# Kernel tuning notes

Hardware: AMD Instinct MI355X
Metric: run time of the kernel (lower is better)

Reference implementation:

```python
import jax, jax.numpy as jnp
import numpy as np

E, S, Q, NN_NODES, R = 2048, 256, 25, 36, 15
H = 128  # MLP hidden width


def setup_inputs() -> dict:
    key = jax.random.key(0)
    ks = jax.random.split(key, 16)
    g = lambda k, shape, scale=1.0: (jax.random.normal(k, shape, dtype=jnp.float32) * scale)
    inp = {
        "nodes": g(ks[0], (E, NN_NODES, 2)),
        "W1": g(ks[1], (2, H), 1.0 / np.sqrt(2.0)),
        "b1": jnp.zeros((H,), jnp.float32),
        "W2": g(ks[2], (H, H), 1.0 / np.sqrt(H)),
        "b2": jnp.zeros((H,), jnp.float32),
        "W3": g(ks[3], (H, H), 1.0 / np.sqrt(H)),
        "b3": jnp.zeros((H,), jnp.float32),
        "W4": g(ks[4], (H, 1), 1.0 / np.sqrt(H)),
        "b4": jnp.zeros((1,), jnp.float32),
        # 2nd-derivative interpolation matrices of the inter basis B at the
        # sub-element quadrature points (shared across big elements).
        "Ixx": g(ks[5], (S, Q, NN_NODES), 0.1),
        "Iyy": g(ks[6], (S, Q, NN_NODES), 0.1),
        # per-big-element 2x2 Hessian change-of-coordinates map (B_DD_inter)
        "B_DD": g(ks[7], (E, 2, 2)),
        "w_quad": jax.random.uniform(ks[8], (Q,), dtype=jnp.float32),
        # test-function values at quadrature points (b.Base)
        "Base": g(ks[9], (Q, R)),
        # per-sub-element Jacobians and precomputed RHS projections F_total
        "J": jax.random.uniform(ks[10], (E, S), dtype=jnp.float32),
        "F": g(ks[11], (E, S, R)),
    }
    return inp


def _mlp(x, W1, b1, W2, b2, W3, b3, W4, b4):
    h = jnp.tanh(x @ W1 + b1)
    h = jnp.tanh(h @ W2 + b2)
    h = jnp.tanh(h @ W3 + b3)
    return h @ W4 + b4


def reference(nodes, W1, b1, W2, b2, W3, b3, W4, b4,
              Ixx, Iyy, B_DD, w_quad, Base, J, F):
    # NN evaluated once per big element at its interpolation nodes: [E, n_nodes]
    ev = _mlp(nodes.reshape(-1, 2), W1, b1, W2, b2, W3, b3, W4, b4)
    ev = ev.reshape(E, NN_NODES)
    d2x = jnp.einsum("sqn,en->esq", Ixx, ev)
    d2y = jnp.einsum("sqn,en->esq", Iyy, ev)
    grad_second = jnp.stack([d2x, d2y], axis=2)           # [E,S,2,Q]
    # B_DD_inter @ grad_second^T, per big element
    grad_second = jnp.einsum("eij,esjq->esiq", B_DD, grad_second)
    integrand_1 = grad_second.sum(axis=2)                 # [E,S,Q]
    # u_NN_el[r] = -J * sum_q w[q] * Base[q,r] * integrand_1[q]
    u_el = -J[:, :, None] * jnp.einsum("q,qr,esq->esr", w_quad, Base, integrand_1)
    res = u_el - F                                        # [E,S,R]
    # loss_element = mean over test functions, summed over all (big, sub) elements
    return jnp.sum(jnp.mean(jnp.square(res), axis=-1))
```

## Files before the change

### kernel.cpp

```cpp
#include <hip/hip_runtime.h>

#define EN 2048
#define SN 256
#define QN 25
#define NNODES 36
#define RN 15
#define HN 128

typedef __attribute__((ext_vector_type(8))) short short8;
typedef __attribute__((ext_vector_type(4))) float f32x4;
typedef __attribute__((ext_vector_type(2))) unsigned int uint2v;

__device__ __forceinline__ unsigned short f2bf(float f) {
    unsigned int u = __float_as_uint(f);
    u += 0x7fffu + ((u >> 16) & 1u);
    return (unsigned short)(u >> 16);
}
__device__ __forceinline__ float bf2f(unsigned short h) {
    return __uint_as_float(((unsigned int)h) << 16);
}
__device__ __forceinline__ float fast_tanh(float x) {
    float xs = x * 2.885390082f;
    xs = fminf(fmaxf(xs, -60.f), 60.f);
    float e = __builtin_amdgcn_exp2f(xs);
    float r = __builtin_amdgcn_rcpf(e + 1.f);
    return fmaf(-2.f, r, 1.f);
}

__global__ void zero_kernel(float* __restrict__ out) {
    if (threadIdx.x == 0) out[0] = 0.f;
}

__global__ __launch_bounds__(256)
void mc_kernel(const float* __restrict__ Ixx, const float* __restrict__ Iyy,
               const float* __restrict__ wq, const float* __restrict__ Base,
               float* __restrict__ Mc)
{
    __shared__ float WB[QN * 16];
    const int t = threadIdx.x;
    for (int i = t; i < QN * 16; i += 256) {
        const int q = i >> 4, r = i & 15;
        if (r < RN) WB[i] = wq[q] * Base[q * RN + r];
    }
    __syncthreads();
    const int o = blockIdx.x * 256 + t;
    const int c  = o % 72;
    const int sr = o / 72;
    const int r  = sr % RN;
    const int s  = sr / RN;
    const float* __restrict__ I = (c < NNODES) ? Ixx : Iyy;
    const int n = (c < NNODES) ? c : (c - NNODES);
    float a0 = 0.f, a1 = 0.f;
    #pragma unroll
    for (int q = 0; q < QN - 1; q += 2) {
        a0 = fmaf(WB[q * 16 + r],       I[(s * QN + q) * NNODES + n],       a0);
        a1 = fmaf(WB[(q + 1) * 16 + r], I[(s * QN + q + 1) * NNODES + n],   a1);
    }
    a0 = fmaf(WB[(QN - 1) * 16 + r], I[(s * QN + QN - 1) * NNODES + n], a0);
    Mc[o] = a0 + a1;
}

__device__ __forceinline__ void load_W(const float* __restrict__ W,
                                       unsigned short (*Ws)[136], int t)
{
    const int n = t & 127;
    const int h = t >> 7;
    #pragma unroll
    for (int kk = 0; kk < 16; kk++) {
        const int k0 = (kk * 2 + h) * 4;
        const float a0 = W[(k0 + 0) * HN + n];
        const float a1 = W[(k0 + 1) * HN + n];
        const float a2 = W[(k0 + 2) * HN + n];
        const float a3 = W[(k0 + 3) * HN + n];
        uint2v pk;
        pk[0] = (unsigned)f2bf(a0) | ((unsigned)f2bf(a1) << 16);
        pk[1] = (unsigned)f2bf(a2) | ((unsigned)f2bf(a3) << 16);
        *(uint2v*)&Ws[n][k0] = pk;
    }
}

__device__ __forceinline__ void mfma_layer(unsigned short (*Hs)[136],
                                           const unsigned short (*Ws)[136],
                                           const float* __restrict__ bias,
                                           int wv, int rowA, int quad)
{
    const int r0 = wv * 32;
    short8 afrag[2][4];
    #pragma unroll
    for (int rt = 0; rt < 2; rt++)
        #pragma unroll
        for (int kt = 0; kt < 4; kt++)
            afrag[rt][kt] = *(const short8*)&Hs[r0 + rt * 16 + rowA][kt * 32 + quad * 8];

    f32x4 acc[2][8];
    const f32x4 zero = {0.f, 0.f, 0.f, 0.f};
    #pragma unroll
    for (int rt = 0; rt < 2; rt++)
        #pragma unroll
        for (int nt = 0; nt < 8; nt++) acc[rt][nt] = zero;

    #pragma unroll
    for (int nt = 0; nt < 8; nt++) {
        #pragma unroll
        for (int kt = 0; kt < 4; kt++) {
            const short8 bfrag = *(const short8*)&Ws[nt * 16 + rowA][kt * 32 + quad * 8];
            acc[0][nt] = __builtin_amdgcn_mfma_f32_16x16x32_bf16(afrag[0][kt], bfrag, acc[0][nt], 0, 0, 0);
            acc[1][nt] = __builtin_amdgcn_mfma_f32_16x16x32_bf16(afrag[1][kt], bfrag, acc[1][nt], 0, 0, 0);
        }
    }
    #pragma unroll
    for (int nt = 0; nt < 8; nt++) {
        const int col = nt * 16 + rowA;
        const float bv = bias[col];
        #pragma unroll
        for (int rt = 0; rt < 2; rt++) {
            #pragma unroll
            for (int rg = 0; rg < 4; rg++) {
                const float v = fast_tanh(acc[rt][nt][rg] + bv);
                Hs[r0 + rt * 16 + quad * 4 + rg][col] = f2bf(v);
            }
        }
    }
}

__global__ __launch_bounds__(256, 2)
void mlp_kernel(const float* __restrict__ nodes,
                const float* __restrict__ W1, const float* __restrict__ b1,
                const float* __restrict__ W2, const float* __restrict__ b2,
                const float* __restrict__ W3, const float* __restrict__ b3,
                const float* __restrict__ W4, const float* __restrict__ b4,
                const float* __restrict__ B_DD,
                float* __restrict__ evc)
{
    __shared__ unsigned short Hs[128][136];
    __shared__ unsigned short Ws[128][136];
    const int t    = threadIdx.x;
    const int lane = t & 63;
    const int wv   = t >> 6;
    const int rowA = lane & 15;
    const int quad = lane >> 4;

    {
        const int p  = t >> 1;
        const int P  = blockIdx.x * 128 + p;
        const float x0 = nodes[2 * P], x1 = nodes[2 * P + 1];
        const int n0 = (t & 1) * 64;
        #pragma unroll
        for (int i = 0; i < 16; i++) {
            const int n = n0 + 4 * i;
            const float4 wa = *(const float4*)(W1 + n);
            const float4 wb = *(const float4*)(W1 + HN + n);
            const float4 bb = *(const float4*)(b1 + n);
            const float h0 = fast_tanh(fmaf(x0, wa.x, fmaf(x1, wb.x, bb.x)));
            const float h1 = fast_tanh(fmaf(x0, wa.y, fmaf(x1, wb.y, bb.y)));
            const float h2 = fast_tanh(fmaf(x0, wa.z, fmaf(x1, wb.z, bb.z)));
            const float h3 = fast_tanh(fmaf(x0, wa.w, fmaf(x1, wb.w, bb.w)));
            uint2v pk;
            pk[0] = (unsigned)f2bf(h0) | ((unsigned)f2bf(h1) << 16);
            pk[1] = (unsigned)f2bf(h2) | ((unsigned)f2bf(h3) << 16);
            *(uint2v*)&Hs[p][n] = pk;
        }
    }
    load_W(W2, Ws, t);
    __syncthreads();
    mfma_layer(Hs, Ws, b2, wv, rowA, quad);
    __syncthreads();
    load_W(W3, Ws, t);
    __syncthreads();
    mfma_layer(Hs, Ws, b3, wv, rowA, quad);
    {
        const int p  = t >> 1;
        const int k0 = (t & 1) * 64;
        float d = 0.f;
        #pragma unroll
        for (int i = 0; i < 8; i++) {
            const short8 h = *(const short8*)&Hs[p][k0 + 8 * i];
            const float4 wA = *(const float4*)(W4 + k0 + 8 * i);
            const float4 wB = *(const float4*)(W4 + k0 + 8 * i + 4);
            d = fmaf(bf2f((unsigned short)h[0]), wA.x, d);
            d = fmaf(bf2f((unsigned short)h[1]), wA.y, d);
            d = fmaf(bf2f((unsigned short)h[2]), wA.z, d);
            d = fmaf(bf2f((unsigned short)h[3]), wA.w, d);
            d = fmaf(bf2f((unsigned short)h[4]), wB.x, d);
            d = fmaf(bf2f((unsigned short)h[5]), wB.y, d);
            d = fmaf(bf2f((unsigned short)h[6]), wB.z, d);
            d = fmaf(bf2f((unsigned short)h[7]), wB.w, d);
        }
        d += __shfl_xor(d, 1, 64);
        if ((t & 1) == 0) {
            const float ev = d + b4[0];
            const int P  = blockIdx.x * 128 + p;
            const int e  = P / NNODES;
            const int ne = P - e * NNODES;
            const float c0 = B_DD[4 * e + 0] + B_DD[4 * e + 2];
            const float c1 = B_DD[4 * e + 1] + B_DD[4 * e + 3];
            evc[e * 72 + ne]      = c0 * ev;
            evc[e * 72 + 36 + ne] = c1 * ev;
        }
    }
}

__global__ __launch_bounds__(256, 2)
void loss_kernel(const float* __restrict__ Mc, const float* __restrict__ evcg,
                 const float* __restrict__ J, const float* __restrict__ F,
                 float* __restrict__ out)
{
    const int t    = threadIdx.x;
    const int lane = t & 63;
    const int wv   = t >> 6;
    const int e0 = (blockIdx.x & 31) * 64;
    const int s0 = (blockIdx.x >> 5) * 4;
    const int e = e0 + lane;
    const int s = __builtin_amdgcn_readfirstlane(s0 + wv);

    float evr[72];
    const float4* ep = (const float4*)(evcg + e * 72);
    #pragma unroll
    for (int i = 0; i < 18; i++) {
        const float4 v = ep[i];
        evr[4 * i + 0] = v.x; evr[4 * i + 1] = v.y;
        evr[4 * i + 2] = v.z; evr[4 * i + 3] = v.w;
    }
    const float Jv = J[e * SN + s];
    const float* __restrict__ Fp = F + (e * SN + s) * RN;
    float Fv[RN];
    #pragma unroll
    for (int r = 0; r < RN; r++) Fv[r] = Fp[r];

    const float* __restrict__ Mb = Mc + s * (RN * 72);
    float acc = 0.f;
    for (int r = 0; r < RN; r++) {
        const float* __restrict__ Mr = Mb + r * 72;
        float d0 = 0.f, d1 = 0.f, d2 = 0.f, d3 = 0.f;
        #pragma unroll
        for (int n = 0; n < 72; n += 4) {
            d0 = fmaf(Mr[n + 0], evr[n + 0], d0);
            d1 = fmaf(Mr[n + 1], evr[n + 1], d1);
            d2 = fmaf(Mr[n + 2], evr[n + 2], d2);
            d3 = fmaf(Mr[n + 3], evr[n + 3], d3);
        }
        const float d = (d0 + d1) + (d2 + d3);
        const float res = fmaf(-Jv, d, -Fv[r]);
        acc = fmaf(res, res, acc);
    }
    acc *= (1.f / (float)RN);
    #pragma unroll
    for (int off = 32; off > 0; off >>= 1)
        acc += __shfl_down(acc, off, 64);
    __shared__ float wsum[4];
    if (lane == 0) wsum[wv] = acc;
    __syncthreads();
    if (t == 0) atomicAdd(out, (wsum[0] + wsum[1]) + (wsum[2] + wsum[3]));
}

extern "C" void kernel_launch(void* const* d_in, const int* in_sizes, int n_in,
                              void* d_out, int out_size, void* d_ws, size_t ws_size,
                              hipStream_t stream)
{
    (void)in_sizes; (void)n_in; (void)out_size; (void)ws_size;
    const float* nodes = (const float*)d_in[0];
    const float* W1   = (const float*)d_in[1];
    const float* b1   = (const float*)d_in[2];
    const float* W2   = (const float*)d_in[3];
    const float* b2   = (const float*)d_in[4];
    const float* W3   = (const float*)d_in[5];
    const float* b3   = (const float*)d_in[6];
    const float* W4   = (const float*)d_in[7];
    const float* b4   = (const float*)d_in[8];
    const float* Ixx  = (const float*)d_in[9];
    const float* Iyy  = (const float*)d_in[10];
    const float* B_DD = (const float*)d_in[11];
    const float* wq   = (const float*)d_in[12];
    const float* Base = (const float*)d_in[13];
    const float* J    = (const float*)d_in[14];
    const float* F    = (const float*)d_in[15];
    float* out = (float*)d_out;
    float* evc = (float*)d_ws;
    float* Mc  = (float*)((char*)d_ws + EN * 72 * sizeof(float));

    zero_kernel<<<1, 64, 0, stream>>>(out);
    mc_kernel<<<1080, 256, 0, stream>>>(Ixx, Iyy, wq, Base, Mc);
    mlp_kernel<<<576, 256, 0, stream>>>(nodes, W1, b1, W2, b2, W3, b3, W4, b4, B_DD, evc);
    loss_kernel<<<2048, 256, 0, stream>>>(Mc, evc, J, F, out);
}
```

Measured before the change: 178.0 us.

## Merge prep kernels into one launch and remap loss kernel to hold Mc rows in registers

The zero, Mc-precompute and MLP kernels become a single launch, with blocks split by block index, which removes two launches and lets the two independent stages overlap. The loss kernel is remapped so each thread handles one (s, r) pair and keeps that Mc row in registers while looping over 16 elements. It reads evc values that are uniform across lanes and masks the padded 16th r lane. This cuts redundant per-thread evc loads and improves F/J coalescing. In exchange, one in sixteen lanes is wasted and F is read with a stride of RN.

```diff
diff --git a/kernel.cpp b/kernel.cpp
--- a/kernel.cpp
+++ b/kernel.cpp
@@ -25,39 +25,6 @@
     float e = __builtin_amdgcn_exp2f(xs);
     float r = __builtin_amdgcn_rcpf(e + 1.f);
     return fmaf(-2.f, r, 1.f);
-}
-
-__global__ void zero_kernel(float* __restrict__ out) {
-    if (threadIdx.x == 0) out[0] = 0.f;
-}
-
-__global__ __launch_bounds__(256)
-void mc_kernel(const float* __restrict__ Ixx, const float* __restrict__ Iyy,
-               const float* __restrict__ wq, const float* __restrict__ Base,
-               float* __restrict__ Mc)
-{
-    __shared__ float WB[QN * 16];
-    const int t = threadIdx.x;
-    for (int i = t; i < QN * 16; i += 256) {
-        const int q = i >> 4, r = i & 15;
-        if (r < RN) WB[i] = wq[q] * Base[q * RN + r];
-    }
-    __syncthreads();
-    const int o = blockIdx.x * 256 + t;
-    const int c  = o % 72;
-    const int sr = o / 72;
-    const int r  = sr % RN;
-    const int s  = sr / RN;
-    const float* __restrict__ I = (c < NNODES) ? Ixx : Iyy;
-    const int n = (c < NNODES) ? c : (c - NNODES);
-    float a0 = 0.f, a1 = 0.f;
-    #pragma unroll
-    for (int q = 0; q < QN - 1; q += 2) {
-        a0 = fmaf(WB[q * 16 + r],       I[(s * QN + q) * NNODES + n],       a0);
-        a1 = fmaf(WB[(q + 1) * 16 + r], I[(s * QN + q + 1) * NNODES + n],   a1);
-    }
-    a0 = fmaf(WB[(QN - 1) * 16 + r], I[(s * QN + QN - 1) * NNODES + n], a0);
-    Mc[o] = a0 + a1;
 }
 
 __device__ __forceinline__ void load_W(const float* __restrict__ W,
@@ -123,131 +90,170 @@
     }
 }
 
+#define MLP_BLOCKS 576
+#define MC_BLOCKS 1080
+
 __global__ __launch_bounds__(256, 2)
-void mlp_kernel(const float* __restrict__ nodes,
-                const float* __restrict__ W1, const float* __restrict__ b1,
-                const float* __restrict__ W2, const float* __restrict__ b2,
-                const float* __restrict__ W3, const float* __restrict__ b3,
-                const float* __restrict__ W4, const float* __restrict__ b4,
-                const float* __restrict__ B_DD,
-                float* __restrict__ evc)
+void prep_kernel(const float* __restrict__ nodes,
+                 const float* __restrict__ W1, const float* __restrict__ b1,
+                 const float* __restrict__ W2, const float* __restrict__ b2,
+                 const float* __restrict__ W3, const float* __restrict__ b3,
+                 const float* __restrict__ W4, const float* __restrict__ b4,
+                 const float* __restrict__ B_DD,
+                 const float* __restrict__ Ixx, const float* __restrict__ Iyy,
+                 const float* __restrict__ wq, const float* __restrict__ Base,
+                 float* __restrict__ evc, float* __restrict__ Mc,
+                 float* __restrict__ out)
 {
     __shared__ unsigned short Hs[128][136];
     __shared__ unsigned short Ws[128][136];
-    const int t    = threadIdx.x;
-    const int lane = t & 63;
-    const int wv   = t >> 6;
-    const int rowA = lane & 15;
-    const int quad = lane >> 4;
-
-    {
-        const int p  = t >> 1;
-        const int P  = blockIdx.x * 128 + p;
-        const float x0 = nodes[2 * P], x1 = nodes[2 * P + 1];
-        const int n0 = (t & 1) * 64;
-        #pragma unroll
-        for (int i = 0; i < 16; i++) {
-            const int n = n0 + 4 * i;
-            const float4 wa = *(const float4*)(W1 + n);
-            const float4 wb = *(const float4*)(W1 + HN + n);
-            const float4 bb = *(const float4*)(b1 + n);
-            const float h0 = fast_tanh(fmaf(x0, wa.x, fmaf(x1, wb.x, bb.x)));
-            const float h1 = fast_tanh(fmaf(x0, wa.y, fmaf(x1, wb.y, bb.y)));
-            const float h2 = fast_tanh(fmaf(x0, wa.z, fmaf(x1, wb.z, bb.z)));
-            const float h3 = fast_tanh(fmaf(x0, wa.w, fmaf(x1, wb.w, bb.w)));
-            uint2v pk;
-            pk[0] = (unsigned)f2bf(h0) | ((unsigned)f2bf(h1) << 16);
-            pk[1] = (unsigned)f2bf(h2) | ((unsigned)f2bf(h3) << 16);
-            *(uint2v*)&Hs[p][n] = pk;
-        }
-    }
-    load_W(W2, Ws, t);
-    __syncthreads();
-    mfma_layer(Hs, Ws, b2, wv, rowA, quad);
-    __syncthreads();
-    load_W(W3, Ws, t);
-    __syncthreads();
-    mfma_layer(Hs, Ws, b3, wv, rowA, quad);
-    {
-        const int p  = t >> 1;
-        const int k0 = (t & 1) * 64;
-        float d = 0.f;
-        #pragma unroll
-        for (int i = 0; i < 8; i++) {
-            const short8 h = *(const short8*)&Hs[p][k0 + 8 * i];
-            const float4 wA = *(const float4*)(W4 + k0 + 8 * i);
-            const float4 wB = *(const float4*)(W4 + k0 + 8 * i + 4);
-            d = fmaf(bf2f((unsigned short)h[0]), wA.x, d);
-            d = fmaf(bf2f((unsigned short)h[1]), wA.y, d);
-            d = fmaf(bf2f((unsigned short)h[2]), wA.z, d);
-            d = fmaf(bf2f((unsigned short)h[3]), wA.w, d);
-            d = fmaf(bf2f((unsigned short)h[4]), wB.x, d);
-            d = fmaf(bf2f((unsigned short)h[5]), wB.y, d);
-            d = fmaf(bf2f((unsigned short)h[6]), wB.z, d);
-            d = fmaf(bf2f((unsigned short)h[7]), wB.w, d);
-        }
-        d += __shfl_xor(d, 1, 64);
-        if ((t & 1) == 0) {
-            const float ev = d + b4[0];
-            const int P  = blockIdx.x * 128 + p;
-            const int e  = P / NNODES;
-            const int ne = P - e * NNODES;
-            const float c0 = B_DD[4 * e + 0] + B_DD[4 * e + 2];
-            const float c1 = B_DD[4 * e + 1] + B_DD[4 * e + 3];
-            evc[e * 72 + ne]      = c0 * ev;
-            evc[e * 72 + 36 + ne] = c1 * ev;
-        }
-    }
-}
-
-__global__ __launch_bounds__(256, 2)
+    __shared__ float WB[QN * 16];
+    const int bid = blockIdx.x;
+    const int t   = threadIdx.x;
+
+    if (bid < MLP_BLOCKS) {
+        const int lane = t & 63;
+        const int wv   = t >> 6;
+        const int rowA = lane & 15;
+        const int quad = lane >> 4;
+
+        {
+            const int p  = t >> 1;
+            const int P  = bid * 128 + p;
+            const float x0 = nodes[2 * P], x1 = nodes[2 * P + 1];
+            const int n0 = (t & 1) * 64;
+            #pragma unroll
+            for (int i = 0; i < 16; i++) {
+                const int n = n0 + 4 * i;
+                const float4 wa = *(const float4*)(W1 + n);
+                const float4 wb = *(const float4*)(W1 + HN + n);
+                const float4 bb = *(const float4*)(b1 + n);
+                const float h0 = fast_tanh(fmaf(x0, wa.x, fmaf(x1, wb.x, bb.x)));
+                const float h1 = fast_tanh(fmaf(x0, wa.y, fmaf(x1, wb.y, bb.y)));
+                const float h2 = fast_tanh(fmaf(x0, wa.z, fmaf(x1, wb.z, bb.z)));
+                const float h3 = fast_tanh(fmaf(x0, wa.w, fmaf(x1, wb.w, bb.w)));
+                uint2v pk;
+                pk[0] = (unsigned)f2bf(h0) | ((unsigned)f2bf(h1) << 16);
+                pk[1] = (unsigned)f2bf(h2) | ((unsigned)f2bf(h3) << 16);
+                *(uint2v*)&Hs[p][n] = pk;
+            }
+        }
+        load_W(W2, Ws, t);
+        __syncthreads();
+        mfma_layer(Hs, Ws, b2, wv, rowA, quad);
+        __syncthreads();
+        load_W(W3, Ws, t);
+        __syncthreads();
+        mfma_layer(Hs, Ws, b3, wv, rowA, quad);
+        {
+            const int p  = t >> 1;
+            const int k0 = (t & 1) * 64;
+            float d = 0.f;
+            #pragma unroll
+            for (int i = 0; i < 8; i++) {
+                const short8 h = *(const short8*)&Hs[p][k0 + 8 * i];
+                const float4 wA = *(const float4*)(W4 + k0 + 8 * i);
+                const float4 wB = *(const float4*)(W4 + k0 + 8 * i + 4);
+                d = fmaf(bf2f((unsigned short)h[0]), wA.x, d);
+                d = fmaf(bf2f((unsigned short)h[1]), wA.y, d);
+                d = fmaf(bf2f((unsigned short)h[2]), wA.z, d);
+                d = fmaf(bf2f((unsigned short)h[3]), wA.w, d);
+                d = fmaf(bf2f((unsigned short)h[4]), wB.x, d);
+                d = fmaf(bf2f((unsigned short)h[5]), wB.y, d);
+                d = fmaf(bf2f((unsigned short)h[6]), wB.z, d);
+                d = fmaf(bf2f((unsigned short)h[7]), wB.w, d);
+            }
+            d += __shfl_xor(d, 1, 64);
+            if ((t & 1) == 0) {
+                const float ev = d + b4[0];
+                const int P  = bid * 128 + p;
+                const int e  = P / NNODES;
+                const int ne = P - e * NNODES;
+                const float c0 = B_DD[4 * e + 0] + B_DD[4 * e + 2];
+                const float c1 = B_DD[4 * e + 1] + B_DD[4 * e + 3];
+                evc[e * 72 + ne]      = c0 * ev;
+                evc[e * 72 + 36 + ne] = c1 * ev;
+            }
+        }
+    } else {
+        if (bid == MLP_BLOCKS && t == 0) out[0] = 0.f;
+        for (int i = t; i < QN * 16; i += 256) {
+            const int q = i >> 4, r = i & 15;
+            if (r < RN) WB[i] = wq[q] * Base[q * RN + r];
+        }
+        __syncthreads();
+        const int o = (bid - MLP_BLOCKS) * 256 + t;
+        const int c  = o % 72;
+        const int sr = o / 72;
+        const int r  = sr % RN;
+        const int s  = sr / RN;
+        const float* __restrict__ I = (c < NNODES) ? Ixx : Iyy;
+        const int n = (c < NNODES) ? c : (c - NNODES);
+        float a0 = 0.f, a1 = 0.f;
+        #pragma unroll
+        for (int q = 0; q < QN - 1; q += 2) {
+            a0 = fmaf(WB[q * 16 + r],       I[(s * QN + q) * NNODES + n],     a0);
+            a1 = fmaf(WB[(q + 1) * 16 + r], I[(s * QN + q + 1) * NNODES + n], a1);
+        }
+        a0 = fmaf(WB[(QN - 1) * 16 + r], I[(s * QN + QN - 1) * NNODES + n], a0);
+        Mc[o] = a0 + a1;
+    }
+}
+
+__global__ __launch_bounds__(256, 4)
 void loss_kernel(const float* __restrict__ Mc, const float* __restrict__ evcg,
                  const float* __restrict__ J, const float* __restrict__ F,
                  float* __restrict__ out)
 {
-    const int t    = threadIdx.x;
-    const int lane = t & 63;
-    const int wv   = t >> 6;
-    const int e0 = (blockIdx.x & 31) * 64;
-    const int s0 = (blockIdx.x >> 5) * 4;
-    const int e = e0 + lane;
-    const int s = __builtin_amdgcn_readfirstlane(s0 + wv);
-
-    float evr[72];
-    const float4* ep = (const float4*)(evcg + e * 72);
-    #pragma unroll
-    for (int i = 0; i < 18; i++) {
-        const float4 v = ep[i];
-        evr[4 * i + 0] = v.x; evr[4 * i + 1] = v.y;
-        evr[4 * i + 2] = v.z; evr[4 * i + 3] = v.w;
-    }
-    const float Jv = J[e * SN + s];
-    const float* __restrict__ Fp = F + (e * SN + s) * RN;
-    float Fv[RN];
-    #pragma unroll
-    for (int r = 0; r < RN; r++) Fv[r] = Fp[r];
-
-    const float* __restrict__ Mb = Mc + s * (RN * 72);
+    const int t  = threadIdx.x;
+    const int r  = t & 15;
+    const int s  = (blockIdx.x & 15) * 16 + (t >> 4);
+    const int e0 = (int)(blockIdx.x >> 4) * 16;
+    const int rr = (r < RN) ? r : (RN - 1);
+    const float vmask = (r < RN) ? 1.f : 0.f;
+
+    float mc[72];
+    {
+        const float4* __restrict__ mp = (const float4*)(Mc + ((size_t)s * RN + rr) * 72);
+        #pragma unroll
+        for (int i = 0; i < 18; i++) {
+            const float4 v = mp[i];
+            mc[4*i+0] = v.x; mc[4*i+1] = v.y; mc[4*i+2] = v.z; mc[4*i+3] = v.w;
+        }
+    }
+
+    const float* __restrict__ Jp = J + (size_t)e0 * SN + s;
+    const float* __restrict__ Fp = F + ((size_t)e0 * SN + s) * RN + rr;
+    const float* __restrict__ ev = evcg + (size_t)e0 * 72;
+
     float acc = 0.f;
-    for (int r = 0; r < RN; r++) {
-        const float* __restrict__ Mr = Mb + r * 72;
+    #pragma unroll 1
+    for (int ei = 0; ei < 16; ei++) {
+        const float Jv = *Jp;
+        const float Fv = *Fp;
         float d0 = 0.f, d1 = 0.f, d2 = 0.f, d3 = 0.f;
         #pragma unroll
         for (int n = 0; n < 72; n += 4) {
-            d0 = fmaf(Mr[n + 0], evr[n + 0], d0);
-            d1 = fmaf(Mr[n + 1], evr[n + 1], d1);
-            d2 = fmaf(Mr[n + 2], evr[n + 2], d2);
-            d3 = fmaf(Mr[n + 3], evr[n + 3], d3);
+            d0 = fmaf(ev[n + 0], mc[n + 0], d0);
+            d1 = fmaf(ev[n + 1], mc[n + 1], d1);
+            d2 = fmaf(ev[n + 2], mc[n + 2], d2);
+            d3 = fmaf(ev[n + 3], mc[n + 3], d3);
         }
         const float d = (d0 + d1) + (d2 + d3);
-        const float res = fmaf(-Jv, d, -Fv[r]);
+        float res = fmaf(-Jv, d, -Fv);
+        res *= vmask;
         acc = fmaf(res, res, acc);
+        Jp += SN;
+        Fp += SN * RN;
+        ev += 72;
     }
     acc *= (1.f / (float)RN);
-    #pragma unroll
-    for (int off = 32; off > 0; off >>= 1)
+
+    #pragma unroll
+    for (int off = 32; off; off >>= 1)
         acc += __shfl_down(acc, off, 64);
     __shared__ float wsum[4];
+    const int lane = t & 63, wv = t >> 6;
     if (lane == 0) wsum[wv] = acc;
     __syncthreads();
     if (t == 0) atomicAdd(out, (wsum[0] + wsum[1]) + (wsum[2] + wsum[3]));
@@ -278,8 +284,8 @@
     float* evc = (float*)d_ws;
     float* Mc  = (float*)((char*)d_ws + EN * 72 * sizeof(float));
 
-    zero_kernel<<<1, 64, 0, stream>>>(out);
-    mc_kernel<<<1080, 256, 0, stream>>>(Ixx, Iyy, wq, Base, Mc);
-    mlp_kernel<<<576, 256, 0, stream>>>(nodes, W1, b1, W2, b2, W3, b3, W4, b4, B_DD, evc);
+    prep_kernel<<<MLP_BLOCKS + MC_BLOCKS, 256, 0, stream>>>(
+        nodes, W1, b1, W2, b2, W3, b3, W4, b4, B_DD, Ixx, Iyy, wq, Base,
+        evc, Mc, out);
     loss_kernel<<<2048, 256, 0, stream>>>(Mc, evc, J, F, out);
 }
```

Measured after the change: 172.6 us. 3.0% less time.
